# Kernel optimization log

Hardware: AMD Instinct MI355X
Metric: run time of the kernel (lower is better)

## Reference

```python
import jax, jax.numpy as jnp
import numpy as np

B, S, H, N, D = 2, 2048, 1024, 16, 64  # batch, seq, hidden, heads, head_size
PAD = -30000.0


def setup_inputs() -> dict:
    key = jax.random.key(0)
    kx, kqkv, kout, krpe = jax.random.split(key, 4)
    x = jax.random.normal(kx, (B, S, H), jnp.float32)
    qkv = jax.random.normal(kqkv, (H, 3, N, D), jnp.float32) * H ** (-0.5)
    out_w = jax.random.normal(kout, (N, D, H), jnp.float32) * (N * D) ** (-0.5)
    # rpe_bias is zero-init in torch; use small randn so the bias path is exercised
    rpe_bias = jax.random.normal(krpe, (N, S), jnp.float32) * 0.02
    return {"x": x, "qkv": qkv, "out_w": out_w, "rpe_bias": rpe_bias}


def reference(x, qkv, out_w, rpe_bias):
    # q, k, v: [B, N, S, D]
    q, k, v = jnp.einsum('bsx,xMnd->Mbnsd', x, qkv)
    s = x.shape[1]
    a = jnp.einsum('bnsd,bntd->bnst', q, k) * q.shape[-1] ** (-0.5)
    # cumulative relative-position bias: bias[n, i, j] = cumsum(rpe)[n, i-j] for i>=j,
    # PAD otherwise (exactly what to_tril produces on the row-broadcast cumsum).
    cum = jnp.cumsum(rpe_bias[:, :s], axis=-1)            # [N, S]
    rel = jnp.arange(s)[:, None] - jnp.arange(s)[None, :]  # [S, S], i - j
    bias = jnp.where(rel >= 0, cum[:, jnp.clip(rel, 0)], PAD)  # [N, S, S]
    a = jax.nn.softmax(a + bias, axis=-1)
    mix = jnp.einsum('bnst,bntd->bnsd', a, v)
    return jnp.einsum('bnsd,ndx->bsx', mix, out_w)
```

## Files before the change

### kernel.cpp

```cpp
#include <hip/hip_runtime.h>
#include <hip/hip_bf16.h>
#include <cstdint>
#include <cstddef>

#define B_   2
#define S_   2048
#define H_   1024
#define NH   16
#define DH   64
#define LOG2E 1.4426950408889634f
#define SCALE2 (0.125f * LOG2E)

typedef __hip_bfloat16 bf16;
typedef short bf16x8 __attribute__((ext_vector_type(8)));
typedef float f32x4 __attribute__((ext_vector_type(4)));

#define MFMA16(a, b, c) __builtin_amdgcn_mfma_f32_16x16x32_bf16((a), (b), (c), 0, 0, 0)

__device__ __forceinline__ void async16(const void* g, void* l) {
  __builtin_amdgcn_global_load_lds(
      (const __attribute__((address_space(1))) void*)g,
      (__attribute__((address_space(3))) void*)l,
      16, 0, 0);
}
__device__ __forceinline__ void async4(const void* g, void* l) {
  __builtin_amdgcn_global_load_lds(
      (const __attribute__((address_space(1))) void*)g,
      (__attribute__((address_space(3))) void*)l,
      4, 0, 0);
}

__device__ __forceinline__ short bf16bits(float v) {
  bf16 t = __float2bfloat16(v);
  return *reinterpret_cast<short*>(&t);
}

__device__ __forceinline__ void tr_body(const float* __restrict__ src,
                                        bf16* __restrict__ dst, int R, int C,
                                        int c0, int r0, bf16 (*tile)[33], int tid) {
  int tx = tid & 31, ty = tid >> 5;
  for (int i = 0; i < 32; i += 8)
    tile[ty + i][tx] = __float2bfloat16(src[(size_t)(r0 + ty + i) * C + c0 + tx]);
  __syncthreads();
  for (int i = 0; i < 32; i += 8)
    dst[(size_t)(c0 + ty + i) * R + r0 + tx] = tile[tx][ty + i];
}

__global__ __launch_bounds__(256)
void prep(const float* __restrict__ x, bf16* __restrict__ xb,
          const float* __restrict__ qkv, bf16* __restrict__ qkvT,
          const float* __restrict__ outw, bf16* __restrict__ outwT,
          const float* __restrict__ rpe, float* __restrict__ cum) {
  __shared__ char pm[2176] __attribute__((aligned(16)));
  const int L = blockIdx.x, tid = threadIdx.x;
  if (L < 4096) {
    int i = (L * 256 + tid) * 4;
    float4 v = *(const float4*)(x + i);
    bf16 o[4] = {__float2bfloat16(v.x), __float2bfloat16(v.y),
                 __float2bfloat16(v.z), __float2bfloat16(v.w)};
    *(uint64_t*)(xb + i) = *(const uint64_t*)o;
  } else if (L < 7168) {
    int t = L - 4096;
    int cx = t % 96, ry = t / 96;
    tr_body(qkv, qkvT, 1024, 3072, cx * 32, ry * 32, (bf16(*)[33])pm, tid);
  } else if (L < 8192) {
    int t = L - 7168;
    int cx = t & 31, ry = t >> 5;
    tr_body(outw, outwT, 1024, 1024, cx * 32, ry * 32, (bf16(*)[33])pm, tid);
  } else {
    float* ssum = (float*)pm;
    int n = L - 8192;
    float loc[8];
    float s = 0.f;
    int base = tid * 8;
#pragma unroll
    for (int u = 0; u < 8; ++u) {
      loc[u] = rpe[n * S_ + base + u];
      s += loc[u];
    }
    ssum[tid] = s;
    __syncthreads();
    float own = s;
    for (int off = 1; off < 256; off <<= 1) {
      float v = (tid >= off) ? ssum[tid - off] : 0.f;
      __syncthreads();
      ssum[tid] += v;
      __syncthreads();
    }
    float run = ssum[tid] - own;
#pragma unroll
    for (int u = 0; u < 8; ++u) {
      run += loc[u];
      cum[n * S_ + base + u] = run * LOG2E;
    }
  }
}

template <int MODE>
__global__ __launch_bounds__(256, MODE == 0 ? 3 : 2)
void gemm_bt(const bf16* __restrict__ A, const bf16* __restrict__ Bt,
             bf16* __restrict__ C0, bf16* __restrict__ C1, bf16* __restrict__ C2,
             float* __restrict__ F0) {
  constexpr int NT = (MODE == 0) ? 4 : 2;
  constexpr int NB = NT * 32;
  __shared__ char smem[MODE == 0 ? 36864 : 12288] __attribute__((aligned(16)));
  bf16* As = (bf16*)smem;
  bf16* Bs = (bf16*)(smem + 8192);
  const int tid = threadIdx.x, lane = tid & 63, w = tid >> 6;
  const int lr = lane & 15, lq = lane >> 4;
  const int m0 = blockIdx.y * 128, n0 = blockIdx.x * NB;
  const int wm = (w & 1) * 64, wn = (w >> 1) * (NT * 16);

  f32x4 acc[4][NT] = {};

  for (int k0 = 0; k0 < 1024; k0 += 32) {
    __syncthreads();
#pragma unroll
    for (int t = 0; t < 2; ++t) {
      int c = (t * 4 + w) * 64 + lane;
      int row = c >> 2, ch = c & 3;
      int k8 = (ch ^ ((row >> 1) & 3)) * 8;
      async16(A + (size_t)(m0 + row) * 1024 + k0 + k8,
              (char*)As + (size_t)(t * 4 + w) * 1024 + lane * 16);
    }
#pragma unroll
    for (int t = 0; t < NB / 64; ++t) {
      int c = (t * 4 + w) * 64 + lane;
      int row = c >> 2, ch = c & 3;
      int k8 = (ch ^ ((row >> 1) & 3)) * 8;
      async16(Bt + (size_t)(n0 + row) * 1024 + k0 + k8,
              (char*)Bs + (size_t)(t * 4 + w) * 1024 + lane * 16);
    }
    __syncthreads();
    bf16x8 af[4], bfr[NT];
#pragma unroll
    for (int mt = 0; mt < 4; ++mt) {
      int row = wm + mt * 16 + lr;
      af[mt] = *(const bf16x8*)(As + row * 32 + ((lq ^ ((row >> 1) & 3)) << 3));
    }
#pragma unroll
    for (int nt = 0; nt < NT; ++nt) {
      int row = wn + nt * 16 + lr;
      bfr[nt] = *(const bf16x8*)(Bs + row * 32 + ((lq ^ ((row >> 1) & 3)) << 3));
    }
#pragma unroll
    for (int mt = 0; mt < 4; ++mt)
#pragma unroll
      for (int nt = 0; nt < NT; ++nt)
        acc[mt][nt] = MFMA16(af[mt], bfr[nt], acc[mt][nt]);
  }

  if (MODE == 0) {
    __syncthreads();
    bf16* E = (bf16*)smem + w * (64 * 72);
    const int cbase = n0 + wn;
    const int mm = cbase >> 10, nn = (cbase >> 6) & 15;
    const int bb = (m0 + wm) >> 11;
    const int sbase = (m0 + wm) & 2047;
    if (mm < 2) {
#pragma unroll
      for (int mt = 0; mt < 4; ++mt)
#pragma unroll
        for (int nt = 0; nt < 4; ++nt)
#pragma unroll
          for (int r = 0; r < 4; ++r)
            E[(mt * 16 + lq * 4 + r) * 72 + nt * 16 + lr] =
                __float2bfloat16(acc[mt][nt][r]);
      bf16* dst = (mm == 0 ? C0 : C1) +
                  ((size_t)(bb * NH + nn) * S_ + sbase) * DH;
#pragma unroll
      for (int it = 0; it < 8; ++it) {
        int c = it * 64 + lane;
        int rw = c >> 3, c8 = c & 7;
        *(uint4*)(dst + (size_t)rw * DH + c8 * 8) =
            *(const uint4*)(E + rw * 72 + c8 * 8);
      }
    } else {
#pragma unroll
      for (int mt = 0; mt < 4; ++mt)
#pragma unroll
        for (int nt = 0; nt < 4; ++nt)
#pragma unroll
          for (int r = 0; r < 4; ++r)
            E[(nt * 16 + lr) * 72 + mt * 16 + lq * 4 + r] =
                __float2bfloat16(acc[mt][nt][r]);
      bf16* dst = C2 + (size_t)(bb * NH + nn) * DH * S_;
#pragma unroll
      for (int it = 0; it < 8; ++it) {
        int c = it * 64 + lane;
        int dr = c >> 3, c8 = c & 7;
        *(uint4*)(dst + (size_t)dr * S_ + sbase + c8 * 8) =
            *(const uint4*)(E + dr * 72 + c8 * 8);
      }
    }
  } else {
#pragma unroll
    for (int mt = 0; mt < 4; ++mt)
#pragma unroll
      for (int nt = 0; nt < NT; ++nt)
#pragma unroll
        for (int r = 0; r < 4; ++r) {
          int rM = m0 + wm + mt * 16 + lq * 4 + r;
          int cN = n0 + wn + nt * 16 + lr;
          F0[(size_t)rM * 1024 + cN] = acc[mt][nt][r];
        }
  }
}

__device__ __forceinline__ void fa_stage(const bf16* __restrict__ k,
                                         const bf16* __restrict__ vt,
                                         const float* __restrict__ cumn,
                                         char* smem, int bn, int i0, int j0,
                                         int buf, int tid) {
  char* dst = smem + buf * 16384;
  const char* ksrc = (const char*)(k + ((size_t)bn * S_ + j0) * DH);
#pragma unroll
  for (int t = 0; t < 2; ++t) {
    int c = t * 256 + tid;
    int row = c >> 3, ch = c & 7;
    int cs = ch ^ ((row & 3) | ((row >> 1) & 4));
    async16(ksrc + row * 128 + cs * 16, dst + c * 16);
  }
  const char* vsrc = (const char*)(vt + (size_t)bn * DH * S_);
#pragma unroll
  for (int t = 0; t < 2; ++t) {
    int c = t * 256 + tid;
    int row = c >> 3, ch = c & 7;
    int cs = ch ^ (row & 7);
    async16(vsrc + (size_t)row * (S_ * 2) + j0 * 2 + cs * 16,
            dst + 8192 + c * 16);
  }
  if (tid < 136) {
    float* cdst = (float*)(smem + 32768) + buf * 544;
    int base = i0 - j0 - 63 + tid;
#pragma unroll
    for (int p = 0; p < 4; ++p) {
      int src = base + p;
      src = src < 0 ? 0 : (src > S_ - 1 ? S_ - 1 : src);
      async4(cumn + src, cdst + p * 136 + tid);
    }
  }
}

__global__ __launch_bounds__(256, 2)
void fa_kernel(const bf16* __restrict__ q, const bf16* __restrict__ k,
               const bf16* __restrict__ vt, const float* __restrict__ cum,
               bf16* __restrict__ mix) {
  __shared__ char smem[37376] __attribute__((aligned(16)));
  float* combL = (float*)(smem + 37120);

  const int tid = threadIdx.x, lane = tid & 63, w = tid >> 6;
  const int lr = lane & 15, lq = lane >> 4;
  const int rg = w & 1, jh = w >> 1;

  const int L = blockIdx.x;
  const int xcd = L & 7, slot = L >> 3;
  const int bn = xcd + 8 * (slot & 3);
  const int pp = slot >> 2;
  const int n = bn & (NH - 1);
  const int b = bn >> 4;
  const float* cumn = cum + n * S_;

  const int T0 = 31 - pp;
  const int T1 = pp;
  const int nu0 = T0 + 1;

  bf16x8 ones;
#pragma unroll
  for (int u = 0; u < 8; ++u) ones[u] = (short)0x3F80;
  const f32x4 fz = {0.f, 0.f, 0.f, 0.f};

  const int kkey = (lr & 3) | (((lr >> 2) & 1) << 2);

  bf16x8 qf[2][2];
  f32x4 oacc[2][4];
  f32x4 lacc[2];

  fa_stage(k, vt, cumn, smem, bn, T0 * 64, 0, 0, tid);

  int ti = T0, jt = 0, i0 = T0 * 64;

  for (int g = 0; g < 33; ++g) {
    const int bsel = g & 1;
    const char* kb = smem + bsel * 16384;
    const char* vb = kb + 8192;
    const float* cumB = (const float*)(smem + 32768) + bsel * 544;
    const int j0 = jt * 64;
    const bool diag = (jt == ti);

    __syncthreads();

    if (g + 1 < 33) {
      int gn = g + 1, tin, jtn;
      if (gn < nu0) { tin = T0; jtn = gn; }
      else          { tin = T1; jtn = gn - nu0; }
      fa_stage(k, vt, cumn, smem, bn, tin * 64, jtn * 64, bsel ^ 1, tid);
    }

    if (jt == 0) {
      const bf16* qbase = q + ((size_t)bn * S_ + i0 + rg * 32) * DH;
#pragma unroll
      for (int is = 0; is < 2; ++is) {
#pragma unroll
        for (int kt = 0; kt < 2; ++kt)
          qf[is][kt] = *(const bf16x8*)(qbase + (is * 16 + lr) * DH + kt * 32 + lq * 8);
        lacc[is] = fz;
#pragma unroll
        for (int dt = 0; dt < 4; ++dt) oacc[is][dt] = fz;
      }
    }

    f32x4 sa[2][2] = {};
#pragma unroll
    for (int kt = 0; kt < 2; ++kt)
#pragma unroll
      for (int nt = 0; nt < 2; ++nt) {
        int krow = jh * 32 + ((lr >> 2) << 3) + nt * 4 + (lr & 3);
        bf16x8 kf = *(const bf16x8*)(kb + krow * 128 +
                        (((kt * 4 + lq) ^ kkey) << 4));
        sa[0][nt] = MFMA16(kf, qf[0][kt], sa[0][nt]);
        sa[1][nt] = MFMA16(kf, qf[1][kt], sa[1][nt]);
      }

    const int doff = i0 - j0;
    bf16x8 pf[2];
#pragma unroll
    for (int is = 0; is < 2; ++is) {
      const int ilocI = rg * 32 + is * 16 + lr;
#pragma unroll
      for (int nt = 0; nt < 2; ++nt) {
        int jl = jh * 32 + lq * 8 + nt * 4;
        int Xm3 = 60 + ilocI - jl;
        int ph = Xm3 & 3, b0 = Xm3 & ~3;
        f32x4 cv = *(const f32x4*)(cumB + ph * 136 + b0);
        if (!diag) {
#pragma unroll
          for (int r = 0; r < 4; ++r)
            pf[is][nt * 4 + r] =
                bf16bits(exp2f(sa[is][nt][r] * SCALE2 + cv[3 - r]));
        } else {
#pragma unroll
          for (int r = 0; r < 4; ++r) {
            float pv = (doff + ilocI - jl - r >= 0)
                           ? exp2f(sa[is][nt][r] * SCALE2 + cv[3 - r])
                           : 0.f;
            pf[is][nt * 4 + r] = bf16bits(pv);
          }
        }
      }
    }

    lacc[0] = MFMA16(pf[0], ones, lacc[0]);
    lacc[1] = MFMA16(pf[1], ones, lacc[1]);
#pragma unroll
    for (int dt = 0; dt < 4; ++dt) {
      int vrow = dt * 16 + lr;
      bf16x8 vf = *(const bf16x8*)(vb + vrow * 128 +
                      (((jh * 4 + lq) ^ (vrow & 7)) << 4));
      oacc[0][dt] = MFMA16(pf[0], vf, oacc[0][dt]);
      oacc[1][dt] = MFMA16(pf[1], vf, oacc[1][dt]);
    }

    if (diag) {
      __syncthreads();
      float* scr = (float*)(smem + bsel * 16384) + rg * 2048;
      if (jh == 1) {
#pragma unroll
        for (int is = 0; is < 2; ++is) {
#pragma unroll
          for (int dt = 0; dt < 4; ++dt)
#pragma unroll
            for (int r = 0; r < 4; ++r) {
              int row = is * 16 + lq * 4 + r;
              int col = ((dt ^ lq) << 4) + lr;
              scr[row * 64 + col] = oacc[is][dt][r];
            }
          if (lr == 0)
#pragma unroll
            for (int r = 0; r < 4; ++r)
              combL[rg * 32 + is * 16 + lq * 4 + r] = lacc[is][r];
        }
      }
      __syncthreads();
      if (jh == 0) {
#pragma unroll
        for (int is = 0; is < 2; ++is) {
#pragma unroll
          for (int r = 0; r < 4; ++r)
            lacc[is][r] += combL[rg * 32 + is * 16 + lq * 4 + r];
#pragma unroll
          for (int dt = 0; dt < 4; ++dt)
#pragma unroll
            for (int r = 0; r < 4; ++r) {
              int row = is * 16 + lq * 4 + r;
              int col = ((dt ^ lq) << 4) + lr;
              oacc[is][dt][r] += scr[row * 64 + col];
            }
        }
#pragma unroll
        for (int is = 0; is < 2; ++is)
#pragma unroll
          for (int dt = 0; dt < 4; ++dt)
#pragma unroll
            for (int r = 0; r < 4; ++r) {
              int i = i0 + rg * 32 + is * 16 + lq * 4 + r;
              int d = dt * 16 + lr;
              mix[((size_t)(b * S_ + i) * NH + n) * DH + d] =
                  __float2bfloat16(oacc[is][dt][r] / lacc[is][r]);
            }
      }
      ti = T1; jt = 0; i0 = T1 * 64;
    } else {
      ++jt;
    }
  }
}

extern "C" void kernel_launch(void* const* d_in, const int* in_sizes, int n_in,
                              void* d_out, int out_size, void* d_ws, size_t ws_size,
                              hipStream_t stream) {
  const float* x     = (const float*)d_in[0];
  const float* qkv   = (const float*)d_in[1];
  const float* out_w = (const float*)d_in[2];
  const float* rpe   = (const float*)d_in[3];
  float* out = (float*)d_out;

  char* ws = (char*)d_ws;
  bf16* qkvT  = (bf16*)(ws + 0);
  bf16* outwT = (bf16*)(ws + 6291456);
  bf16* xb    = (bf16*)(ws + 8388608);
  bf16* qb    = (bf16*)(ws + 16777216);
  bf16* kb    = (bf16*)(ws + 25165824);
  bf16* vtb   = (bf16*)(ws + 33554432);
  bf16* mixb  = (bf16*)(ws + 41943040);
  float* cum  = (float*)(ws + 50331648);

  prep<<<8208, 256, 0, stream>>>(x, xb, qkv, qkvT, out_w, outwT, rpe, cum);
  gemm_bt<0><<<dim3(3072 / 128, 4096 / 128), 256, 0, stream>>>(xb, qkvT, qb, kb, vtb, nullptr);
  fa_kernel<<<512, 256, 0, stream>>>(qb, kb, vtb, cum, mixb);
  gemm_bt<1><<<dim3(1024 / 64, 4096 / 128), 256, 0, stream>>>(mixb, outwT, nullptr, nullptr, nullptr, out);
}
```

Baseline: 182.4 us.

## Double K-tile depth in GEMM and KV tile width in flash attention

The GEMM main loop now stages 64-wide K slices instead of 32, with a new 8-way XOR swizzle, so each barrier pair feeds twice as many MFMAs. The attention kernel processes 128-key blocks per iteration instead of 64, halving the number of pipeline stages and syncs per row-tile pair, and enlarges the bias/cum staging window to match. This costs more LDS (about 72KB in attention), which may limit occupancy to fewer blocks per CU, and it adds masked wasted work on the diagonal block.

```diff
diff --git a/kernel.cpp b/kernel.cpp
--- a/kernel.cpp
+++ b/kernel.cpp
@@ -103,9 +103,9 @@
              float* __restrict__ F0) {
   constexpr int NT = (MODE == 0) ? 4 : 2;
   constexpr int NB = NT * 32;
-  __shared__ char smem[MODE == 0 ? 36864 : 12288] __attribute__((aligned(16)));
+  __shared__ char smem[MODE == 0 ? 36864 : 24576] __attribute__((aligned(16)));
   bf16* As = (bf16*)smem;
-  bf16* Bs = (bf16*)(smem + 8192);
+  bf16* Bs = (bf16*)(smem + 16384);
   const int tid = threadIdx.x, lane = tid & 63, w = tid >> 6;
   const int lr = lane & 15, lq = lane >> 4;
   const int m0 = blockIdx.y * 128, n0 = blockIdx.x * NB;
@@ -113,41 +113,49 @@
 
   f32x4 acc[4][NT] = {};
 
-  for (int k0 = 0; k0 < 1024; k0 += 32) {
+  for (int k0 = 0; k0 < 1024; k0 += 64) {
     __syncthreads();
 #pragma unroll
-    for (int t = 0; t < 2; ++t) {
-      int c = (t * 4 + w) * 64 + lane;
-      int row = c >> 2, ch = c & 3;
-      int k8 = (ch ^ ((row >> 1) & 3)) * 8;
-      async16(A + (size_t)(m0 + row) * 1024 + k0 + k8,
-              (char*)As + (size_t)(t * 4 + w) * 1024 + lane * 16);
-    }
-#pragma unroll
-    for (int t = 0; t < NB / 64; ++t) {
-      int c = (t * 4 + w) * 64 + lane;
-      int row = c >> 2, ch = c & 3;
-      int k8 = (ch ^ ((row >> 1) & 3)) * 8;
-      async16(Bt + (size_t)(n0 + row) * 1024 + k0 + k8,
-              (char*)Bs + (size_t)(t * 4 + w) * 1024 + lane * 16);
+    for (int t = 0; t < 4; ++t) {
+      int c = t * 256 + tid;
+      int row = c >> 3, ch = c & 7;
+      int cs = ch ^ (row & 7);
+      async16(A + (size_t)(m0 + row) * 1024 + k0 + cs * 8,
+              (char*)As + c * 16);
+    }
+#pragma unroll
+    for (int t = 0; t < NB / 32; ++t) {
+      int c = t * 256 + tid;
+      int row = c >> 3, ch = c & 7;
+      int cs = ch ^ (row & 7);
+      async16(Bt + (size_t)(n0 + row) * 1024 + k0 + cs * 8,
+              (char*)Bs + c * 16);
     }
     __syncthreads();
-    bf16x8 af[4], bfr[NT];
+    bf16x8 af[4][2], bfr[NT][2];
 #pragma unroll
     for (int mt = 0; mt < 4; ++mt) {
       int row = wm + mt * 16 + lr;
-      af[mt] = *(const bf16x8*)(As + row * 32 + ((lq ^ ((row >> 1) & 3)) << 3));
+#pragma unroll
+      for (int kt = 0; kt < 2; ++kt)
+        af[mt][kt] = *(const bf16x8*)(As + row * 64 +
+                         (((kt * 4 + lq) ^ (row & 7)) << 3));
     }
 #pragma unroll
     for (int nt = 0; nt < NT; ++nt) {
       int row = wn + nt * 16 + lr;
-      bfr[nt] = *(const bf16x8*)(Bs + row * 32 + ((lq ^ ((row >> 1) & 3)) << 3));
+#pragma unroll
+      for (int kt = 0; kt < 2; ++kt)
+        bfr[nt][kt] = *(const bf16x8*)(Bs + row * 64 +
+                          (((kt * 4 + lq) ^ (row & 7)) << 3));
     }
 #pragma unroll
     for (int mt = 0; mt < 4; ++mt)
 #pragma unroll
       for (int nt = 0; nt < NT; ++nt)
-        acc[mt][nt] = MFMA16(af[mt], bfr[nt], acc[mt][nt]);
+#pragma unroll
+        for (int kt = 0; kt < 2; ++kt)
+          acc[mt][nt] = MFMA16(af[mt][kt], bfr[nt][kt], acc[mt][nt]);
   }
 
   if (MODE == 0) {
@@ -210,12 +218,12 @@
 __device__ __forceinline__ void fa_stage(const bf16* __restrict__ k,
                                          const bf16* __restrict__ vt,
                                          const float* __restrict__ cumn,
-                                         char* smem, int bn, int i0, int j0,
+                                         char* smem, int bn, int i0, int jb,
                                          int buf, int tid) {
-  char* dst = smem + buf * 16384;
-  const char* ksrc = (const char*)(k + ((size_t)bn * S_ + j0) * DH);
-#pragma unroll
-  for (int t = 0; t < 2; ++t) {
+  char* dst = smem + buf * 32768;
+  const char* ksrc = (const char*)(k + ((size_t)bn * S_ + jb) * DH);
+#pragma unroll
+  for (int t = 0; t < 4; ++t) {
     int c = t * 256 + tid;
     int row = c >> 3, ch = c & 7;
     int cs = ch ^ ((row & 3) | ((row >> 1) & 4));
@@ -223,21 +231,21 @@
   }
   const char* vsrc = (const char*)(vt + (size_t)bn * DH * S_);
 #pragma unroll
-  for (int t = 0; t < 2; ++t) {
+  for (int t = 0; t < 4; ++t) {
     int c = t * 256 + tid;
-    int row = c >> 3, ch = c & 7;
-    int cs = ch ^ (row & 7);
-    async16(vsrc + (size_t)row * (S_ * 2) + j0 * 2 + cs * 16,
-            dst + 8192 + c * 16);
-  }
-  if (tid < 136) {
-    float* cdst = (float*)(smem + 32768) + buf * 544;
-    int base = i0 - j0 - 63 + tid;
+    int row = c >> 4, ch = c & 15;
+    int cs = ch ^ (row & 15);
+    async16(vsrc + (size_t)row * (S_ * 2) + jb * 2 + cs * 16,
+            dst + 16384 + c * 16);
+  }
+  if (tid < 194) {
+    float* cdst = (float*)(smem + 65536) + buf * 800;
+    int base = i0 - jb - 127 + tid;
 #pragma unroll
     for (int p = 0; p < 4; ++p) {
       int src = base + p;
       src = src < 0 ? 0 : (src > S_ - 1 ? S_ - 1 : src);
-      async4(cumn + src, cdst + p * 136 + tid);
+      async4(cumn + src, cdst + p * 200 + tid);
     }
   }
 }
@@ -246,8 +254,8 @@
 void fa_kernel(const bf16* __restrict__ q, const bf16* __restrict__ k,
                const bf16* __restrict__ vt, const float* __restrict__ cum,
                bf16* __restrict__ mix) {
-  __shared__ char smem[37376] __attribute__((aligned(16)));
-  float* combL = (float*)(smem + 37120);
+  __shared__ char smem[72192] __attribute__((aligned(16)));
+  float* combL = (float*)(smem + 71936);
 
   const int tid = threadIdx.x, lane = tid & 63, w = tid >> 6;
   const int lr = lane & 15, lq = lane >> 4;
@@ -263,7 +271,7 @@
 
   const int T0 = 31 - pp;
   const int T1 = pp;
-  const int nu0 = T0 + 1;
+  const int nu0 = (T0 + 2) >> 1;
 
   bf16x8 ones;
 #pragma unroll
@@ -278,23 +286,23 @@
 
   fa_stage(k, vt, cumn, smem, bn, T0 * 64, 0, 0, tid);
 
-  int ti = T0, jt = 0, i0 = T0 * 64;
-
-  for (int g = 0; g < 33; ++g) {
+  int ti = T0, jt = 0, i0 = T0 * 64, nu = nu0;
+
+  for (int g = 0; g < 17; ++g) {
     const int bsel = g & 1;
-    const char* kb = smem + bsel * 16384;
-    const char* vb = kb + 8192;
-    const float* cumB = (const float*)(smem + 32768) + bsel * 544;
-    const int j0 = jt * 64;
-    const bool diag = (jt == ti);
+    const char* kb = smem + bsel * 32768;
+    const char* vb = kb + 16384;
+    const float* cumB = (const float*)(smem + 65536) + bsel * 800;
+    const int jb = jt * 128;
+    const bool diag = (jt == nu - 1);
 
     __syncthreads();
 
-    if (g + 1 < 33) {
+    if (g + 1 < 17) {
       int gn = g + 1, tin, jtn;
       if (gn < nu0) { tin = T0; jtn = gn; }
       else          { tin = T1; jtn = gn - nu0; }
-      fa_stage(k, vt, cumn, smem, bn, tin * 64, jtn * 64, bsel ^ 1, tid);
+      fa_stage(k, vt, cumn, smem, bn, tin * 64, jtn * 128, bsel ^ 1, tid);
     }
 
     if (jt == 0) {
@@ -302,68 +310,73 @@
 #pragma unroll
       for (int is = 0; is < 2; ++is) {
 #pragma unroll
-        for (int kt = 0; kt < 2; ++kt)
-          qf[is][kt] = *(const bf16x8*)(qbase + (is * 16 + lr) * DH + kt * 32 + lq * 8);
+        for (int kd = 0; kd < 2; ++kd)
+          qf[is][kd] = *(const bf16x8*)(qbase + (is * 16 + lr) * DH + kd * 32 + lq * 8);
         lacc[is] = fz;
 #pragma unroll
         for (int dt = 0; dt < 4; ++dt) oacc[is][dt] = fz;
       }
     }
 
-    f32x4 sa[2][2] = {};
-#pragma unroll
-    for (int kt = 0; kt < 2; ++kt)
-#pragma unroll
-      for (int nt = 0; nt < 2; ++nt) {
-        int krow = jh * 32 + ((lr >> 2) << 3) + nt * 4 + (lr & 3);
+    f32x4 sa[2][4] = {};
+#pragma unroll
+    for (int kd = 0; kd < 2; ++kd)
+#pragma unroll
+      for (int mm = 0; mm < 4; ++mm) {
+        int kt = mm >> 1, nt2 = mm & 1;
+        int krow = jh * 64 + kt * 32 + ((lr >> 2) << 3) + nt2 * 4 + (lr & 3);
         bf16x8 kf = *(const bf16x8*)(kb + krow * 128 +
-                        (((kt * 4 + lq) ^ kkey) << 4));
-        sa[0][nt] = MFMA16(kf, qf[0][kt], sa[0][nt]);
-        sa[1][nt] = MFMA16(kf, qf[1][kt], sa[1][nt]);
-      }
-
-    const int doff = i0 - j0;
-    bf16x8 pf[2];
+                        (((kd * 4 + lq) ^ kkey) << 4));
+        sa[0][mm] = MFMA16(kf, qf[0][kd], sa[0][mm]);
+        sa[1][mm] = MFMA16(kf, qf[1][kd], sa[1][mm]);
+      }
+
+    const int doff = i0 - jb;
+    bf16x8 pf[2][2];
 #pragma unroll
     for (int is = 0; is < 2; ++is) {
       const int ilocI = rg * 32 + is * 16 + lr;
 #pragma unroll
-      for (int nt = 0; nt < 2; ++nt) {
-        int jl = jh * 32 + lq * 8 + nt * 4;
-        int Xm3 = 60 + ilocI - jl;
+      for (int mm = 0; mm < 4; ++mm) {
+        int kt = mm >> 1, nt2 = mm & 1;
+        int jl = jh * 64 + kt * 32 + lq * 8 + nt2 * 4;
+        int Xm3 = 124 + ilocI - jl;
         int ph = Xm3 & 3, b0 = Xm3 & ~3;
-        f32x4 cv = *(const f32x4*)(cumB + ph * 136 + b0);
+        f32x4 cv = *(const f32x4*)(cumB + ph * 200 + b0);
         if (!diag) {
 #pragma unroll
           for (int r = 0; r < 4; ++r)
-            pf[is][nt * 4 + r] =
-                bf16bits(exp2f(sa[is][nt][r] * SCALE2 + cv[3 - r]));
+            pf[is][kt][nt2 * 4 + r] =
+                bf16bits(exp2f(sa[is][mm][r] * SCALE2 + cv[3 - r]));
         } else {
 #pragma unroll
           for (int r = 0; r < 4; ++r) {
             float pv = (doff + ilocI - jl - r >= 0)
-                           ? exp2f(sa[is][nt][r] * SCALE2 + cv[3 - r])
+                           ? exp2f(sa[is][mm][r] * SCALE2 + cv[3 - r])
                            : 0.f;
-            pf[is][nt * 4 + r] = bf16bits(pv);
+            pf[is][kt][nt2 * 4 + r] = bf16bits(pv);
           }
         }
       }
     }
 
-    lacc[0] = MFMA16(pf[0], ones, lacc[0]);
-    lacc[1] = MFMA16(pf[1], ones, lacc[1]);
-#pragma unroll
-    for (int dt = 0; dt < 4; ++dt) {
-      int vrow = dt * 16 + lr;
-      bf16x8 vf = *(const bf16x8*)(vb + vrow * 128 +
-                      (((jh * 4 + lq) ^ (vrow & 7)) << 4));
-      oacc[0][dt] = MFMA16(pf[0], vf, oacc[0][dt]);
-      oacc[1][dt] = MFMA16(pf[1], vf, oacc[1][dt]);
+#pragma unroll
+    for (int kt = 0; kt < 2; ++kt) {
+      lacc[0] = MFMA16(pf[0][kt], ones, lacc[0]);
+      lacc[1] = MFMA16(pf[1][kt], ones, lacc[1]);
+#pragma unroll
+      for (int dt = 0; dt < 4; ++dt) {
+        int vrow = dt * 16 + lr;
+        bf16x8 vf = *(const bf16x8*)(vb + vrow * 256 +
+                        (((jh * 8 + kt * 4 + lq) ^ (vrow & 15)) << 4));
+        oacc[0][dt] = MFMA16(pf[0][kt], vf, oacc[0][dt]);
+        oacc[1][dt] = MFMA16(pf[1][kt], vf, oacc[1][dt]);
+      }
     }
 
     if (diag) {
       __syncthreads();
-      float* scr = (float*)(smem + bsel * 16384) + rg * 2048;
+      float* scr = (float*)(smem + bsel * 32768) + rg * 2048;
       if (jh == 1) {
 #pragma unroll
         for (int is = 0; is < 2; ++is) {
@@ -409,7 +422,7 @@
                   __float2bfloat16(oacc[is][dt][r] / lacc[is][r]);
             }
       }
-      ti = T1; jt = 0; i0 = T1 * 64;
+      ti = T1; jt = 0; i0 = T1 * 64; nu = (T1 + 2) >> 1;
     } else {
       ++jt;
     }
```

Measured after the change: 178.5 us. -2.1%, faster.
